# Kernel optimization log

Hardware: AMD Instinct MI355X
Metric: run time of the kernel (lower is better)

## Reference

```python
import jax, jax.numpy as jnp
import numpy as np

N = 100000      # nodes
E = 1600000     # edges (avg degree 16)
D_IN = 128
D_OUT = 128
P = 0.5         # dropout prob (module is in training mode)


def setup_inputs() -> dict:
    key = jax.random.key(0)
    k1, k2, k3 = jax.random.split(key, 3)
    x = jax.random.normal(k1, (N, D_IN), dtype=jnp.float32)
    edge_index = jax.random.randint(k2, (2, E), 0, N, dtype=jnp.int32)
    # GCNConv learned params (glorot-ish weight, zero bias)
    weight = jax.random.normal(k3, (D_IN, D_OUT), dtype=jnp.float32) / np.float32(np.sqrt(D_IN))
    bias = jnp.zeros((D_OUT,), dtype=jnp.float32)
    return {"x": x, "edge_index": edge_index, "weight": weight, "bias": bias}


def reference(x, edge_index, weight, bias):
    # --- GCNConv: add self-loops, symmetric deg^-1/2 normalization ---
    loops = jnp.arange(N, dtype=edge_index.dtype)
    src = jnp.concatenate([edge_index[0], loops])   # [E+N]
    dst = jnp.concatenate([edge_index[1], loops])   # [E+N]
    deg = jax.ops.segment_sum(jnp.ones_like(dst, dtype=x.dtype), dst, num_segments=N)
    dinv = jnp.where(deg > 0, jax.lax.rsqrt(deg), 0.0)          # deg^-1/2
    norm = dinv[src] * dinv[dst]                                # [E+N]
    h = x @ weight                                              # [N, D_OUT]
    msgs = h[src] * norm[:, None]                               # gather + scale
    out = jax.ops.segment_sum(msgs, dst, num_segments=N) + bias # scatter-add
    # --- ReLU ---
    out = jax.nn.relu(out)
    # --- Dropout (training=True), fixed key for determinism ---
    keep = jax.random.bernoulli(jax.random.key(42), 1.0 - P, out.shape)
    return jnp.where(keep, out / (1.0 - P), jnp.zeros((), out.dtype))
```

## Files before the change

### kernel.cpp

```cpp
#include <hip/hip_runtime.h>

#define N_NODES 100000
#define E_EDGES 1600000
#define D 128
#define PAD 136
#define GEMM_BLKS 1563
#define CCHUNK 4096
#define CNT_BLKS ((E_EDGES + CCHUNK - 1) / CCHUNK)
#define SCHUNK 4096
#define SCAT_BLKS ((E_EDGES + SCHUNK - 1) / SCHUNK)
#define RANGE 98
#define NR 1024
#define CAP 2048
#define NPW 13

typedef __attribute__((ext_vector_type(8))) short short8;
typedef __attribute__((ext_vector_type(8))) unsigned short ushort8v;
typedef __attribute__((ext_vector_type(4))) float f32x4;

__device__ __forceinline__ unsigned int rotl32(unsigned int x, int r) {
  return (x << r) | (x >> (32 - r));
}

__device__ __forceinline__ unsigned int threefry_bits(unsigned int ctr) {
  const unsigned int ks0 = 0u, ks1 = 42u;
  const unsigned int ks2 = ks0 ^ ks1 ^ 0x1BD11BDAu;
  unsigned int x0 = ks0;
  unsigned int x1 = ctr + ks1;
#define TF_ROUND(R) { x0 += x1; x1 = rotl32(x1, R); x1 ^= x0; }
  TF_ROUND(13) TF_ROUND(15) TF_ROUND(26) TF_ROUND(6)
  x0 += ks1; x1 += ks2 + 1u;
  TF_ROUND(17) TF_ROUND(29) TF_ROUND(16) TF_ROUND(24)
  x0 += ks2; x1 += ks0 + 2u;
  TF_ROUND(13) TF_ROUND(15) TF_ROUND(26) TF_ROUND(6)
  x0 += ks0; x1 += ks1 + 3u;
  TF_ROUND(17) TF_ROUND(29) TF_ROUND(16) TF_ROUND(24)
  x0 += ks1; x1 += ks2 + 4u;
  TF_ROUND(13) TF_ROUND(15) TF_ROUND(26) TF_ROUND(6)
  x0 += ks2; x1 += ks0 + 5u;
#undef TF_ROUND
  return x0 ^ x1;
}

__device__ __forceinline__ unsigned short f2bf(float f) {
  unsigned int u = __float_as_uint(f);
  u = (u + 0x7FFFu + ((u >> 16) & 1u)) >> 16;
  return (unsigned short)u;
}
__device__ __forceinline__ float bf2f_lo(unsigned int v) {
  return __uint_as_float(v << 16);
}
__device__ __forceinline__ float bf2f_hi(unsigned int v) {
  return __uint_as_float(v & 0xFFFF0000u);
}

__global__ __launch_bounds__(256) void k_init(const float* __restrict__ w,
                                              unsigned short* __restrict__ wbf,
                                              int* __restrict__ bnt) {
  int t = blockIdx.x * 256 + threadIdx.x;
  if (t < 128 * 128) {
    int k = t >> 7;
    int n = t & 127;
    wbf[n * 128 + k] = f2bf(w[t]);
  }
  if (t < NR) bnt[t] = 0;
}

__global__ __launch_bounds__(256) void k_gc(const float* __restrict__ x,
                                            const unsigned short* __restrict__ wbf,
                                            unsigned short* __restrict__ h,
                                            const int* __restrict__ ei,
                                            int* __restrict__ bnt) {
  __shared__ unsigned short Wl[128 * PAD];
  __shared__ unsigned short Xl[64 * PAD];
  const int t = threadIdx.x;

  if (blockIdx.x >= GEMM_BLKS) {
    int* lc = (int*)Xl;
    const int base = (blockIdx.x - GEMM_BLKS) * CCHUNK;
    for (int i = t; i < NR; i += 256) lc[i] = 0;
    __syncthreads();
#pragma unroll
    for (int i = 0; i < CCHUNK / 256; ++i) {
      int e = base + i * 256 + t;
      if (e < E_EDGES) {
        int d = ei[E_EDGES + e];
        atomicAdd(&lc[d / RANGE], 1);
      }
    }
    __syncthreads();
    for (int i = t; i < NR; i += 256) {
      int c = lc[i];
      if (c) atomicAdd(&bnt[i], c);
    }
    return;
  }

  const int row0 = blockIdx.x * 64;

#pragma unroll
  for (int i = 0; i < 8; ++i) {
    int u  = t + i * 256;
    int kg = u & 15;
    int n  = u >> 4;
    *(ushort8v*)&Wl[n * PAD + kg * 8] = *(const ushort8v*)&wbf[n * 128 + kg * 8];
  }
  const float4* x4 = (const float4*)x;
#pragma unroll
  for (int i = 0; i < 8; ++i) {
    int id = t + i * 256;
    int r  = id >> 5;
    int c4 = id & 31;
    int row = row0 + r; if (row >= N_NODES) row = N_NODES - 1;
    float4 v = x4[(long long)row * 32 + c4];
    ushort4 p;
    p.x = f2bf(v.x); p.y = f2bf(v.y); p.z = f2bf(v.z); p.w = f2bf(v.w);
    *(ushort4*)&Xl[r * PAD + c4 * 4] = p;
  }
  __syncthreads();

  const int wv   = t >> 6;
  const int l    = t & 63;
  const int quad = l >> 4;
  const int ln16 = l & 15;
  const int m0   = wv * 16;

  short8 a[4];
#pragma unroll
  for (int kt = 0; kt < 4; ++kt)
    a[kt] = *(const short8*)&Xl[(m0 + ln16) * PAD + kt * 32 + quad * 8];

#pragma unroll
  for (int nt = 0; nt < 8; ++nt) {
    f32x4 acc = {0.f, 0.f, 0.f, 0.f};
#pragma unroll
    for (int kt = 0; kt < 4; ++kt) {
      short8 b = *(const short8*)&Wl[(nt * 16 + ln16) * PAD + kt * 32 + quad * 8];
      acc = __builtin_amdgcn_mfma_f32_16x16x32_bf16(a[kt], b, acc, 0, 0, 0);
    }
#pragma unroll
    for (int r = 0; r < 4; ++r)
      Xl[(m0 + quad * 4 + r) * PAD + nt * 16 + ln16] = f2bf(acc[r]);
  }

#pragma unroll
  for (int v = 0; v < 4; ++v) {
    int idx = v * 64 + l;
    int rr  = idx >> 4;
    int ch  = idx & 15;
    int row = row0 + m0 + rr;
    if (row < N_NODES)
      *(ushort8v*)&h[(long long)row * D + ch * 8] = *(const ushort8v*)&Xl[(m0 + rr) * PAD + ch * 8];
  }
}

__global__ __launch_bounds__(1024) void k_scanb(const int* __restrict__ bnt,
                                                int* __restrict__ base,
                                                int* __restrict__ cur) {
  __shared__ int sm[NR];
  int t = threadIdx.x;
  int v = bnt[t];
  sm[t] = v;
  __syncthreads();
  for (int off = 1; off < NR; off <<= 1) {
    int x = (t >= off) ? sm[t - off] : 0;
    __syncthreads();
    sm[t] += x;
    __syncthreads();
  }
  int excl = sm[t] - v;
  base[t] = excl;
  cur[t]  = excl;
  if (t == NR - 1) base[NR] = sm[NR - 1];
}

__global__ __launch_bounds__(512) void k_scatter(const int* __restrict__ ei,
                                                 int* __restrict__ cur,
                                                 int* __restrict__ ebuf) {
  __shared__ int lcnt[NR];
  __shared__ int gbase[NR];
  const int t = threadIdx.x;
  const int base = blockIdx.x * SCHUNK;
  for (int i = t; i < NR; i += 512) lcnt[i] = 0;
  __syncthreads();
  int myb[SCHUNK / 512];
  int myr[SCHUNK / 512];
  int mypk[SCHUNK / 512];
#pragma unroll
  for (int i = 0; i < SCHUNK / 512; ++i) {
    int e = base + i * 512 + t;
    myb[i] = -1;
    if (e < E_EDGES) {
      int d = ei[E_EDGES + e];
      int s = ei[e];
      int b = d / RANGE;
      int dl = d - b * RANGE;
      myb[i]  = b;
      mypk[i] = s | (dl << 17);
      myr[i]  = atomicAdd(&lcnt[b], 1);
    }
  }
  __syncthreads();
  for (int i = t; i < NR; i += 512) {
    int c = lcnt[i];
    gbase[i] = c ? atomicAdd(&cur[i], c) : 0;
  }
  __syncthreads();
#pragma unroll
  for (int i = 0; i < SCHUNK / 512; ++i)
    if (myb[i] >= 0) ebuf[gbase[myb[i]] + myr[i]] = mypk[i];
}

__global__ __launch_bounds__(256) void k_deg(const int* __restrict__ ebuf,
                                             const int* __restrict__ base,
                                             float* __restrict__ dinv) {
  __shared__ int hist[RANGE];
  const int t = threadIdx.x;
  const int r = blockIdx.x;
  if (t < RANGE) hist[t] = 0;
  __syncthreads();
  const int lo = base[r], hi = base[r + 1];
  for (int e = lo + t; e < hi; e += 256)
    atomicAdd(&hist[((unsigned)ebuf[e]) >> 17], 1);
  __syncthreads();
  if (t < RANGE) {
    int n = r * RANGE + t;
    if (n < N_NODES) dinv[n] = rsqrtf((float)(hist[t] + 1));
  }
}

__global__ __launch_bounds__(512) void k_agg(const int* __restrict__ ebuf,
                                             const int* __restrict__ base,
                                             const float* __restrict__ dinv,
                                             const unsigned short* __restrict__ h,
                                             const float* __restrict__ bias,
                                             float* __restrict__ out) {
  __shared__ int ssort[CAP];
  __shared__ int shist[128];
  __shared__ int sscn[128];
  __shared__ int scur[128];
  const int t  = threadIdx.x;
  const int r  = blockIdx.x;
  const int wv = t >> 6;
  const int l  = t & 63;
  const unsigned int* h32 = (const unsigned int*)h;

  float a0[NPW], a1[NPW];
#pragma unroll
  for (int j = 0; j < NPW; ++j) { a0[j] = 0.f; a1[j] = 0.f; }

  const int lo = base[r], hi = base[r + 1];

  for (int c0 = lo; c0 < hi; c0 += CAP) {
    const int m = min(CAP, hi - c0);
    if (t < 128) shist[t] = 0;
    __syncthreads();

    int pk0 = -1, pk1 = -1, pk2 = -1, pk3 = -1;
    {
      int i0 = t, i1 = t + 512, i2 = t + 1024, i3 = t + 1536;
      if (i0 < m) { pk0 = ebuf[c0 + i0]; atomicAdd(&shist[((unsigned)pk0) >> 17], 1); }
      if (i1 < m) { pk1 = ebuf[c0 + i1]; atomicAdd(&shist[((unsigned)pk1) >> 17], 1); }
      if (i2 < m) { pk2 = ebuf[c0 + i2]; atomicAdd(&shist[((unsigned)pk2) >> 17], 1); }
      if (i3 < m) { pk3 = ebuf[c0 + i3]; atomicAdd(&shist[((unsigned)pk3) >> 17], 1); }
    }
    __syncthreads();

    if (t < 128) sscn[t] = shist[t];
    __syncthreads();
    for (int off = 1; off < 128; off <<= 1) {
      int xv = (t < 128 && t >= off) ? sscn[t - off] : 0;
      __syncthreads();
      if (t < 128) sscn[t] += xv;
      __syncthreads();
    }
    if (t < 128) scur[t] = sscn[t] - shist[t];
    __syncthreads();

    if (pk0 != -1) ssort[atomicAdd(&scur[((unsigned)pk0) >> 17], 1)] = pk0;
    if (pk1 != -1) ssort[atomicAdd(&scur[((unsigned)pk1) >> 17], 1)] = pk1;
    if (pk2 != -1) ssort[atomicAdd(&scur[((unsigned)pk2) >> 17], 1)] = pk2;
    if (pk3 != -1) ssort[atomicAdd(&scur[((unsigned)pk3) >> 17], 1)] = pk3;
    __syncthreads();

#pragma unroll
    for (int j = 0; j < NPW; ++j) {
      int nl = wv + 8 * j;
      if (nl < RANGE) {
        int s1i = sscn[nl];
        int s0i = s1i - shist[nl];
        float aa0 = a0[j], aa1 = a1[j];
#pragma unroll 4
        for (int e = s0i; e < s1i; ++e) {
          int p = ssort[e];
          int s = p & 0x1FFFF;
          float wgt = dinv[s];
          unsigned u = h32[(long long)s * 64 + l];
          aa0 = fmaf(bf2f_lo(u), wgt, aa0);
          aa1 = fmaf(bf2f_hi(u), wgt, aa1);
        }
        a0[j] = aa0; a1[j] = aa1;
      }
    }
    __syncthreads();
  }

#pragma unroll
  for (int j = 0; j < NPW; ++j) {
    int nl = wv + 8 * j;
    if (nl >= RANGE) continue;
    int n = r * RANGE + nl;
    if (n >= N_NODES) continue;
    float dv = dinv[n];
    unsigned hv = h32[(long long)n * 64 + l];
    float v0 = (a0[j] + bf2f_lo(hv) * dv) * dv;
    float v1 = (a1[j] + bf2f_hi(hv) * dv) * dv;
    float2 bb = ((const float2*)bias)[l];
    float r0 = fmaxf(v0 + bb.x, 0.f);
    float r1 = fmaxf(v1 + bb.y, 0.f);
    unsigned i0 = (unsigned)n * 128u + (unsigned)(2 * l);
    unsigned b0 = threefry_bits(i0);
    unsigned b1 = threefry_bits(i0 + 1u);
    float2 res;
    res.x = (b0 & 0x80000000u) ? 0.0f : r0 * 2.0f;
    res.y = (b1 & 0x80000000u) ? 0.0f : r1 * 2.0f;
    ((float2*)out)[(long long)n * 64 + l] = res;
  }
}

extern "C" void kernel_launch(void* const* d_in, const int* in_sizes, int n_in,
                              void* d_out, int out_size, void* d_ws, size_t ws_size,
                              hipStream_t stream) {
  const float* x    = (const float*)d_in[0];
  const int*   ei   = (const int*)d_in[1];
  const float* w    = (const float*)d_in[2];
  const float* bias = (const float*)d_in[3];
  float* out = (float*)d_out;

  char* p = (char*)d_ws;
  unsigned short* h   = (unsigned short*)p;  p += (size_t)N_NODES * D * 2;
  unsigned short* wbf = (unsigned short*)p;  p += 128 * 128 * 2;
  float* dinv = (float*)p;                   p += (size_t)(NR * RANGE) * 4;
  int* bnt    = (int*)p;                     p += NR * 4;
  int* base   = (int*)p;                     p += (NR + 4) * 4;
  int* cur    = (int*)p;                     p += NR * 4;
  int* ebuf   = (int*)p;                     p += (size_t)E_EDGES * 4;

  k_init<<<64, 256, 0, stream>>>(w, wbf, bnt);
  k_gc<<<GEMM_BLKS + CNT_BLKS, 256, 0, stream>>>(x, wbf, h, ei, bnt);
  k_scanb<<<1, NR, 0, stream>>>(bnt, base, cur);
  k_scatter<<<SCAT_BLKS, 512, 0, stream>>>(ei, cur, ebuf);
  k_deg<<<NR, 256, 0, stream>>>(ebuf, base, dinv);
  k_agg<<<NR, 512, 0, stream>>>(ebuf, base, dinv, h, bias, out);
}
```

Measured before the change: 246.6 us.

## Halve node bucket range, pad bucket counters, and shrink aggregation blocks

Node buckets shrink from 98 to 49 nodes, so there are twice as many buckets (2048). The aggregation kernel now uses 256-thread blocks with a 1024-entry sort buffer, giving more, smaller blocks for better load balance and occupancy. Global bucket counters are padded to a 16-int stride so atomics on different buckets no longer share a cache line. The sort buffer also stores pre-masked source indices so the inner loop skips the mask. The costs are more global atomics per counting block, and a scan that now handles two buckets per thread.

```diff
diff --git a/kernel.cpp b/kernel.cpp
--- a/kernel.cpp
+++ b/kernel.cpp
@@ -9,10 +9,11 @@
 #define CNT_BLKS ((E_EDGES + CCHUNK - 1) / CCHUNK)
 #define SCHUNK 4096
 #define SCAT_BLKS ((E_EDGES + SCHUNK - 1) / SCHUNK)
-#define RANGE 98
-#define NR 1024
-#define CAP 2048
+#define RANGE 49
+#define NR 2048
+#define CAP 1024
 #define NPW 13
+#define BST 16
 
 typedef __attribute__((ext_vector_type(8))) short short8;
 typedef __attribute__((ext_vector_type(8))) unsigned short ushort8v;
@@ -63,7 +64,7 @@
     int n = t & 127;
     wbf[n * 128 + k] = f2bf(w[t]);
   }
-  if (t < NR) bnt[t] = 0;
+  for (int i = t; i < NR * BST; i += 64 * 256) bnt[i] = 0;
 }
 
 __global__ __launch_bounds__(256) void k_gc(const float* __restrict__ x,
@@ -91,7 +92,7 @@
     __syncthreads();
     for (int i = t; i < NR; i += 256) {
       int c = lc[i];
-      if (c) atomicAdd(&bnt[i], c);
+      if (c) atomicAdd(&bnt[i * BST], c);
     }
     return;
   }
@@ -157,21 +158,25 @@
 __global__ __launch_bounds__(1024) void k_scanb(const int* __restrict__ bnt,
                                                 int* __restrict__ base,
                                                 int* __restrict__ cur) {
-  __shared__ int sm[NR];
+  __shared__ int sm[1024];
   int t = threadIdx.x;
-  int v = bnt[t];
-  sm[t] = v;
-  __syncthreads();
-  for (int off = 1; off < NR; off <<= 1) {
+  int v0 = bnt[(2 * t) * BST];
+  int v1 = bnt[(2 * t + 1) * BST];
+  int s = v0 + v1;
+  sm[t] = s;
+  __syncthreads();
+  for (int off = 1; off < 1024; off <<= 1) {
     int x = (t >= off) ? sm[t - off] : 0;
     __syncthreads();
     sm[t] += x;
     __syncthreads();
   }
-  int excl = sm[t] - v;
-  base[t] = excl;
-  cur[t]  = excl;
-  if (t == NR - 1) base[NR] = sm[NR - 1];
+  int excl = sm[t] - s;
+  base[2 * t]     = excl;
+  base[2 * t + 1] = excl + v0;
+  cur[(2 * t) * BST]     = excl;
+  cur[(2 * t + 1) * BST] = excl + v0;
+  if (t == 1023) base[NR] = sm[1023];
 }
 
 __global__ __launch_bounds__(512) void k_scatter(const int* __restrict__ ei,
@@ -203,7 +208,7 @@
   __syncthreads();
   for (int i = t; i < NR; i += 512) {
     int c = lcnt[i];
-    gbase[i] = c ? atomicAdd(&cur[i], c) : 0;
+    gbase[i] = c ? atomicAdd(&cur[i * BST], c) : 0;
   }
   __syncthreads();
 #pragma unroll
@@ -214,10 +219,10 @@
 __global__ __launch_bounds__(256) void k_deg(const int* __restrict__ ebuf,
                                              const int* __restrict__ base,
                                              float* __restrict__ dinv) {
-  __shared__ int hist[RANGE];
+  __shared__ int hist[64];
   const int t = threadIdx.x;
   const int r = blockIdx.x;
-  if (t < RANGE) hist[t] = 0;
+  if (t < 64) hist[t] = 0;
   __syncthreads();
   const int lo = base[r], hi = base[r + 1];
   for (int e = lo + t; e < hi; e += 256)
@@ -229,16 +234,16 @@
   }
 }
 
-__global__ __launch_bounds__(512) void k_agg(const int* __restrict__ ebuf,
+__global__ __launch_bounds__(256) void k_agg(const int* __restrict__ ebuf,
                                              const int* __restrict__ base,
                                              const float* __restrict__ dinv,
                                              const unsigned short* __restrict__ h,
                                              const float* __restrict__ bias,
                                              float* __restrict__ out) {
   __shared__ int ssort[CAP];
-  __shared__ int shist[128];
-  __shared__ int sscn[128];
-  __shared__ int scur[128];
+  __shared__ int shist[64];
+  __shared__ int sscn[64];
+  __shared__ int scur[64];
   const int t  = threadIdx.x;
   const int r  = blockIdx.x;
   const int wv = t >> 6;
@@ -253,12 +258,12 @@
 
   for (int c0 = lo; c0 < hi; c0 += CAP) {
     const int m = min(CAP, hi - c0);
-    if (t < 128) shist[t] = 0;
+    if (t < 64) shist[t] = 0;
     __syncthreads();
 
     int pk0 = -1, pk1 = -1, pk2 = -1, pk3 = -1;
     {
-      int i0 = t, i1 = t + 512, i2 = t + 1024, i3 = t + 1536;
+      int i0 = t, i1 = t + 256, i2 = t + 512, i3 = t + 768;
       if (i0 < m) { pk0 = ebuf[c0 + i0]; atomicAdd(&shist[((unsigned)pk0) >> 17], 1); }
       if (i1 < m) { pk1 = ebuf[c0 + i1]; atomicAdd(&shist[((unsigned)pk1) >> 17], 1); }
       if (i2 < m) { pk2 = ebuf[c0 + i2]; atomicAdd(&shist[((unsigned)pk2) >> 17], 1); }
@@ -266,34 +271,33 @@
     }
     __syncthreads();
 
-    if (t < 128) sscn[t] = shist[t];
-    __syncthreads();
-    for (int off = 1; off < 128; off <<= 1) {
-      int xv = (t < 128 && t >= off) ? sscn[t - off] : 0;
+    if (t < 64) sscn[t] = shist[t];
+    __syncthreads();
+    for (int off = 1; off < 64; off <<= 1) {
+      int xv = (t < 64 && t >= off) ? sscn[t - off] : 0;
       __syncthreads();
-      if (t < 128) sscn[t] += xv;
+      if (t < 64) sscn[t] += xv;
       __syncthreads();
     }
-    if (t < 128) scur[t] = sscn[t] - shist[t];
-    __syncthreads();
-
-    if (pk0 != -1) ssort[atomicAdd(&scur[((unsigned)pk0) >> 17], 1)] = pk0;
-    if (pk1 != -1) ssort[atomicAdd(&scur[((unsigned)pk1) >> 17], 1)] = pk1;
-    if (pk2 != -1) ssort[atomicAdd(&scur[((unsigned)pk2) >> 17], 1)] = pk2;
-    if (pk3 != -1) ssort[atomicAdd(&scur[((unsigned)pk3) >> 17], 1)] = pk3;
+    if (t < 64) scur[t] = sscn[t] - shist[t];
+    __syncthreads();
+
+    if (pk0 != -1) ssort[atomicAdd(&scur[((unsigned)pk0) >> 17], 1)] = pk0 & 0x1FFFF;
+    if (pk1 != -1) ssort[atomicAdd(&scur[((unsigned)pk1) >> 17], 1)] = pk1 & 0x1FFFF;
+    if (pk2 != -1) ssort[atomicAdd(&scur[((unsigned)pk2) >> 17], 1)] = pk2 & 0x1FFFF;
+    if (pk3 != -1) ssort[atomicAdd(&scur[((unsigned)pk3) >> 17], 1)] = pk3 & 0x1FFFF;
     __syncthreads();
 
 #pragma unroll
     for (int j = 0; j < NPW; ++j) {
-      int nl = wv + 8 * j;
+      int nl = wv + 4 * j;
       if (nl < RANGE) {
         int s1i = sscn[nl];
         int s0i = s1i - shist[nl];
         float aa0 = a0[j], aa1 = a1[j];
 #pragma unroll 4
         for (int e = s0i; e < s1i; ++e) {
-          int p = ssort[e];
-          int s = p & 0x1FFFF;
+          int s = ssort[e];
           float wgt = dinv[s];
           unsigned u = h32[(long long)s * 64 + l];
           aa0 = fmaf(bf2f_lo(u), wgt, aa0);
@@ -307,7 +311,7 @@
 
 #pragma unroll
   for (int j = 0; j < NPW; ++j) {
-    int nl = wv + 8 * j;
+    int nl = wv + 4 * j;
     if (nl >= RANGE) continue;
     int n = r * RANGE + nl;
     if (n >= N_NODES) continue;
@@ -341,15 +345,15 @@
   unsigned short* h   = (unsigned short*)p;  p += (size_t)N_NODES * D * 2;
   unsigned short* wbf = (unsigned short*)p;  p += 128 * 128 * 2;
   float* dinv = (float*)p;                   p += (size_t)(NR * RANGE) * 4;
-  int* bnt    = (int*)p;                     p += NR * 4;
+  int* bnt    = (int*)p;                     p += (size_t)NR * BST * 4;
   int* base   = (int*)p;                     p += (NR + 4) * 4;
-  int* cur    = (int*)p;                     p += NR * 4;
+  int* cur    = (int*)p;                     p += (size_t)NR * BST * 4;
   int* ebuf   = (int*)p;                     p += (size_t)E_EDGES * 4;
 
   k_init<<<64, 256, 0, stream>>>(w, wbf, bnt);
   k_gc<<<GEMM_BLKS + CNT_BLKS, 256, 0, stream>>>(x, wbf, h, ei, bnt);
-  k_scanb<<<1, NR, 0, stream>>>(bnt, base, cur);
+  k_scanb<<<1, 1024, 0, stream>>>(bnt, base, cur);
   k_scatter<<<SCAT_BLKS, 512, 0, stream>>>(ei, cur, ebuf);
   k_deg<<<NR, 256, 0, stream>>>(ebuf, base, dinv);
-  k_agg<<<NR, 512, 0, stream>>>(ebuf, base, dinv, h, bias, out);
-}
+  k_agg<<<NR, 256, 0, stream>>>(ebuf, base, dinv, h, bias, out);
+}
```

Result: slower. 287.5 us (+16.6%).

## Use deterministic per-block bucket offsets and pre-gather dinv weights into LDS

Applied to the files above, without the earlier changes.

Replaces the global atomic bucket counters with a per-block count matrix that is exclusive-scanned per bucket, so the scatter gets deterministic write offsets without global atomics. The counting blocks move to the front of the combined GEMM/count grid. In aggregation, each edge's dinv[src] weight is loaded once during the histogram pass and stored next to the source index in LDS, which takes a dependent global load out of the inner gather loop; that loop's unroll goes from 4 to 8. The cost is an extra serial scan kernel that walks 391 rows of counts, plus twice the LDS per sorted entry.

```diff
diff --git a/kernel.cpp b/kernel.cpp
--- a/kernel.cpp
+++ b/kernel.cpp
@@ -5,10 +5,8 @@
 #define D 128
 #define PAD 136
 #define GEMM_BLKS 1563
-#define CCHUNK 4096
-#define CNT_BLKS ((E_EDGES + CCHUNK - 1) / CCHUNK)
-#define SCHUNK 4096
-#define SCAT_BLKS ((E_EDGES + SCHUNK - 1) / SCHUNK)
+#define CHUNK 4096
+#define CNT_BLKS ((E_EDGES + CHUNK - 1) / CHUNK)
 #define RANGE 98
 #define NR 1024
 #define CAP 2048
@@ -55,33 +53,30 @@
 }
 
 __global__ __launch_bounds__(256) void k_init(const float* __restrict__ w,
-                                              unsigned short* __restrict__ wbf,
-                                              int* __restrict__ bnt) {
+                                              unsigned short* __restrict__ wbf) {
   int t = blockIdx.x * 256 + threadIdx.x;
-  if (t < 128 * 128) {
-    int k = t >> 7;
-    int n = t & 127;
-    wbf[n * 128 + k] = f2bf(w[t]);
-  }
-  if (t < NR) bnt[t] = 0;
+  int k = t >> 7;
+  int n = t & 127;
+  wbf[n * 128 + k] = f2bf(w[t]);
 }
 
 __global__ __launch_bounds__(256) void k_gc(const float* __restrict__ x,
                                             const unsigned short* __restrict__ wbf,
                                             unsigned short* __restrict__ h,
                                             const int* __restrict__ ei,
-                                            int* __restrict__ bnt) {
+                                            int* __restrict__ cnt) {
   __shared__ unsigned short Wl[128 * PAD];
   __shared__ unsigned short Xl[64 * PAD];
   const int t = threadIdx.x;
 
-  if (blockIdx.x >= GEMM_BLKS) {
+  if (blockIdx.x < CNT_BLKS) {
     int* lc = (int*)Xl;
-    const int base = (blockIdx.x - GEMM_BLKS) * CCHUNK;
+    const int B = blockIdx.x;
+    const int base = B * CHUNK;
     for (int i = t; i < NR; i += 256) lc[i] = 0;
     __syncthreads();
 #pragma unroll
-    for (int i = 0; i < CCHUNK / 256; ++i) {
+    for (int i = 0; i < CHUNK / 256; ++i) {
       int e = base + i * 256 + t;
       if (e < E_EDGES) {
         int d = ei[E_EDGES + e];
@@ -89,14 +84,11 @@
       }
     }
     __syncthreads();
-    for (int i = t; i < NR; i += 256) {
-      int c = lc[i];
-      if (c) atomicAdd(&bnt[i], c);
-    }
+    for (int i = t; i < NR; i += 256) cnt[B * NR + i] = lc[i];
     return;
   }
 
-  const int row0 = blockIdx.x * 64;
+  const int row0 = (blockIdx.x - CNT_BLKS) * 64;
 
 #pragma unroll
   for (int i = 0; i < 8; ++i) {
@@ -154,12 +146,24 @@
   }
 }
 
-__global__ __launch_bounds__(1024) void k_scanb(const int* __restrict__ bnt,
-                                                int* __restrict__ base,
-                                                int* __restrict__ cur) {
+__global__ __launch_bounds__(256) void k_scanA(int* __restrict__ cnt,
+                                               int* __restrict__ tot) {
+  const int b = blockIdx.x * 256 + threadIdx.x;
+  int running = 0;
+#pragma unroll 4
+  for (int B = 0; B < CNT_BLKS; ++B) {
+    int v = cnt[B * NR + b];
+    cnt[B * NR + b] = running;
+    running += v;
+  }
+  tot[b] = running;
+}
+
+__global__ __launch_bounds__(1024) void k_scanB(const int* __restrict__ tot,
+                                                int* __restrict__ base) {
   __shared__ int sm[NR];
   int t = threadIdx.x;
-  int v = bnt[t];
+  int v = tot[t];
   sm[t] = v;
   __syncthreads();
   for (int off = 1; off < NR; off <<= 1) {
@@ -168,27 +172,27 @@
     sm[t] += x;
     __syncthreads();
   }
-  int excl = sm[t] - v;
-  base[t] = excl;
-  cur[t]  = excl;
+  base[t] = sm[t] - v;
   if (t == NR - 1) base[NR] = sm[NR - 1];
 }
 
 __global__ __launch_bounds__(512) void k_scatter(const int* __restrict__ ei,
-                                                 int* __restrict__ cur,
+                                                 const int* __restrict__ cnt,
+                                                 const int* __restrict__ base,
                                                  int* __restrict__ ebuf) {
   __shared__ int lcnt[NR];
   __shared__ int gbase[NR];
   const int t = threadIdx.x;
-  const int base = blockIdx.x * SCHUNK;
+  const int B = blockIdx.x;
+  const int e0 = B * CHUNK;
   for (int i = t; i < NR; i += 512) lcnt[i] = 0;
   __syncthreads();
-  int myb[SCHUNK / 512];
-  int myr[SCHUNK / 512];
-  int mypk[SCHUNK / 512];
-#pragma unroll
-  for (int i = 0; i < SCHUNK / 512; ++i) {
-    int e = base + i * 512 + t;
+  int myb[CHUNK / 512];
+  int myr[CHUNK / 512];
+  int mypk[CHUNK / 512];
+#pragma unroll
+  for (int i = 0; i < CHUNK / 512; ++i) {
+    int e = e0 + i * 512 + t;
     myb[i] = -1;
     if (e < E_EDGES) {
       int d = ei[E_EDGES + e];
@@ -201,23 +205,21 @@
     }
   }
   __syncthreads();
-  for (int i = t; i < NR; i += 512) {
-    int c = lcnt[i];
-    gbase[i] = c ? atomicAdd(&cur[i], c) : 0;
-  }
-  __syncthreads();
-#pragma unroll
-  for (int i = 0; i < SCHUNK / 512; ++i)
+  for (int i = t; i < NR; i += 512)
+    gbase[i] = base[i] + cnt[B * NR + i];
+  __syncthreads();
+#pragma unroll
+  for (int i = 0; i < CHUNK / 512; ++i)
     if (myb[i] >= 0) ebuf[gbase[myb[i]] + myr[i]] = mypk[i];
 }
 
 __global__ __launch_bounds__(256) void k_deg(const int* __restrict__ ebuf,
                                              const int* __restrict__ base,
                                              float* __restrict__ dinv) {
-  __shared__ int hist[RANGE];
+  __shared__ int hist[128];
   const int t = threadIdx.x;
   const int r = blockIdx.x;
-  if (t < RANGE) hist[t] = 0;
+  if (t < 128) hist[t] = 0;
   __syncthreads();
   const int lo = base[r], hi = base[r + 1];
   for (int e = lo + t; e < hi; e += 256)
@@ -235,7 +237,7 @@
                                              const unsigned short* __restrict__ h,
                                              const float* __restrict__ bias,
                                              float* __restrict__ out) {
-  __shared__ int ssort[CAP];
+  __shared__ int2 sswp[CAP];
   __shared__ int shist[128];
   __shared__ int sscn[128];
   __shared__ int scur[128];
@@ -257,12 +259,13 @@
     __syncthreads();
 
     int pk0 = -1, pk1 = -1, pk2 = -1, pk3 = -1;
+    float w0 = 0.f, w1 = 0.f, w2 = 0.f, w3 = 0.f;
     {
       int i0 = t, i1 = t + 512, i2 = t + 1024, i3 = t + 1536;
-      if (i0 < m) { pk0 = ebuf[c0 + i0]; atomicAdd(&shist[((unsigned)pk0) >> 17], 1); }
-      if (i1 < m) { pk1 = ebuf[c0 + i1]; atomicAdd(&shist[((unsigned)pk1) >> 17], 1); }
-      if (i2 < m) { pk2 = ebuf[c0 + i2]; atomicAdd(&shist[((unsigned)pk2) >> 17], 1); }
-      if (i3 < m) { pk3 = ebuf[c0 + i3]; atomicAdd(&shist[((unsigned)pk3) >> 17], 1); }
+      if (i0 < m) { pk0 = ebuf[c0 + i0]; w0 = dinv[pk0 & 0x1FFFF]; atomicAdd(&shist[((unsigned)pk0) >> 17], 1); }
+      if (i1 < m) { pk1 = ebuf[c0 + i1]; w1 = dinv[pk1 & 0x1FFFF]; atomicAdd(&shist[((unsigned)pk1) >> 17], 1); }
+      if (i2 < m) { pk2 = ebuf[c0 + i2]; w2 = dinv[pk2 & 0x1FFFF]; atomicAdd(&shist[((unsigned)pk2) >> 17], 1); }
+      if (i3 < m) { pk3 = ebuf[c0 + i3]; w3 = dinv[pk3 & 0x1FFFF]; atomicAdd(&shist[((unsigned)pk3) >> 17], 1); }
     }
     __syncthreads();
 
@@ -277,10 +280,10 @@
     if (t < 128) scur[t] = sscn[t] - shist[t];
     __syncthreads();
 
-    if (pk0 != -1) ssort[atomicAdd(&scur[((unsigned)pk0) >> 17], 1)] = pk0;
-    if (pk1 != -1) ssort[atomicAdd(&scur[((unsigned)pk1) >> 17], 1)] = pk1;
-    if (pk2 != -1) ssort[atomicAdd(&scur[((unsigned)pk2) >> 17], 1)] = pk2;
-    if (pk3 != -1) ssort[atomicAdd(&scur[((unsigned)pk3) >> 17], 1)] = pk3;
+    if (pk0 != -1) sswp[atomicAdd(&scur[((unsigned)pk0) >> 17], 1)] = make_int2(pk0 & 0x1FFFF, __float_as_int(w0));
+    if (pk1 != -1) sswp[atomicAdd(&scur[((unsigned)pk1) >> 17], 1)] = make_int2(pk1 & 0x1FFFF, __float_as_int(w1));
+    if (pk2 != -1) sswp[atomicAdd(&scur[((unsigned)pk2) >> 17], 1)] = make_int2(pk2 & 0x1FFFF, __float_as_int(w2));
+    if (pk3 != -1) sswp[atomicAdd(&scur[((unsigned)pk3) >> 17], 1)] = make_int2(pk3 & 0x1FFFF, __float_as_int(w3));
     __syncthreads();
 
 #pragma unroll
@@ -290,12 +293,11 @@
         int s1i = sscn[nl];
         int s0i = s1i - shist[nl];
         float aa0 = a0[j], aa1 = a1[j];
-#pragma unroll 4
+#pragma unroll 8
         for (int e = s0i; e < s1i; ++e) {
-          int p = ssort[e];
-          int s = p & 0x1FFFF;
-          float wgt = dinv[s];
-          unsigned u = h32[(long long)s * 64 + l];
+          int2 p = sswp[e];
+          float wgt = __int_as_float(p.y);
+          unsigned u = h32[(long long)p.x * 64 + l];
           aa0 = fmaf(bf2f_lo(u), wgt, aa0);
           aa1 = fmaf(bf2f_hi(u), wgt, aa1);
         }
@@ -341,15 +343,16 @@
   unsigned short* h   = (unsigned short*)p;  p += (size_t)N_NODES * D * 2;
   unsigned short* wbf = (unsigned short*)p;  p += 128 * 128 * 2;
   float* dinv = (float*)p;                   p += (size_t)(NR * RANGE) * 4;
-  int* bnt    = (int*)p;                     p += NR * 4;
+  int* cnt    = (int*)p;                     p += (size_t)CNT_BLKS * NR * 4;
+  int* tot    = (int*)p;                     p += NR * 4;
   int* base   = (int*)p;                     p += (NR + 4) * 4;
-  int* cur    = (int*)p;                     p += NR * 4;
   int* ebuf   = (int*)p;                     p += (size_t)E_EDGES * 4;
 
-  k_init<<<64, 256, 0, stream>>>(w, wbf, bnt);
-  k_gc<<<GEMM_BLKS + CNT_BLKS, 256, 0, stream>>>(x, wbf, h, ei, bnt);
-  k_scanb<<<1, NR, 0, stream>>>(bnt, base, cur);
-  k_scatter<<<SCAT_BLKS, 512, 0, stream>>>(ei, cur, ebuf);
+  k_init<<<64, 256, 0, stream>>>(w, wbf);
+  k_gc<<<GEMM_BLKS + CNT_BLKS, 256, 0, stream>>>(x, wbf, h, ei, cnt);
+  k_scanA<<<4, 256, 0, stream>>>(cnt, tot);
+  k_scanB<<<1, NR, 0, stream>>>(tot, base);
+  k_scatter<<<CNT_BLKS, 512, 0, stream>>>(ei, cnt, base, ebuf);
   k_deg<<<NR, 256, 0, stream>>>(ebuf, base, dinv);
   k_agg<<<NR, 512, 0, stream>>>(ebuf, base, dinv, h, bias, out);
 }
```

Result: slower. 288.4 us (+17.0%).

## Bucket edges by source octant and destination, prefetch dinv weights into shared

Applied to the files above, without the earlier changes.

The aggregation kernel now sorts each chunk of edges into 1024 buckets keyed by source-node octant and local destination node. Each block walks the octants in a staggered order starting from blockIdx&7, so concurrently running blocks gather h rows from different regions, which is meant to improve L2 locality of the gathers. The per-edge dinv[src] lookup moves into the load phase and is stored alongside the source index in shared memory. In exchange the scan widens to 1024 bins, shared memory use grows, and the per-node inner loop is split across eight octant passes with shorter trip counts and no unroll pragma.

```diff
diff --git a/kernel.cpp b/kernel.cpp
--- a/kernel.cpp
+++ b/kernel.cpp
@@ -13,6 +13,8 @@
 #define NR 1024
 #define CAP 2048
 #define NPW 13
+#define NB 1024
+#define OCTN 12500
 
 typedef __attribute__((ext_vector_type(8))) short short8;
 typedef __attribute__((ext_vector_type(8))) unsigned short ushort8v;
@@ -214,10 +216,10 @@
 __global__ __launch_bounds__(256) void k_deg(const int* __restrict__ ebuf,
                                              const int* __restrict__ base,
                                              float* __restrict__ dinv) {
-  __shared__ int hist[RANGE];
+  __shared__ int hist[128];
   const int t = threadIdx.x;
   const int r = blockIdx.x;
-  if (t < RANGE) hist[t] = 0;
+  if (t < 128) hist[t] = 0;
   __syncthreads();
   const int lo = base[r], hi = base[r + 1];
   for (int e = lo + t; e < hi; e += 256)
@@ -235,14 +237,15 @@
                                              const unsigned short* __restrict__ h,
                                              const float* __restrict__ bias,
                                              float* __restrict__ out) {
-  __shared__ int ssort[CAP];
-  __shared__ int shist[128];
-  __shared__ int sscn[128];
-  __shared__ int scur[128];
+  __shared__ int2 sswp[CAP];
+  __shared__ int shist[NB];
+  __shared__ int sscn[NB];
+  __shared__ int scur[NB];
   const int t  = threadIdx.x;
   const int r  = blockIdx.x;
   const int wv = t >> 6;
   const int l  = t & 63;
+  const int ostart = blockIdx.x & 7;
   const unsigned int* h32 = (const unsigned int*)h;
 
   float a0[NPW], a1[NPW];
@@ -253,53 +256,68 @@
 
   for (int c0 = lo; c0 < hi; c0 += CAP) {
     const int m = min(CAP, hi - c0);
-    if (t < 128) shist[t] = 0;
+    shist[t] = 0; shist[t + 512] = 0;
     __syncthreads();
 
     int pk0 = -1, pk1 = -1, pk2 = -1, pk3 = -1;
+    int bk0 = 0, bk1 = 0, bk2 = 0, bk3 = 0;
+    float w0 = 0.f, w1 = 0.f, w2 = 0.f, w3 = 0.f;
     {
       int i0 = t, i1 = t + 512, i2 = t + 1024, i3 = t + 1536;
-      if (i0 < m) { pk0 = ebuf[c0 + i0]; atomicAdd(&shist[((unsigned)pk0) >> 17], 1); }
-      if (i1 < m) { pk1 = ebuf[c0 + i1]; atomicAdd(&shist[((unsigned)pk1) >> 17], 1); }
-      if (i2 < m) { pk2 = ebuf[c0 + i2]; atomicAdd(&shist[((unsigned)pk2) >> 17], 1); }
-      if (i3 < m) { pk3 = ebuf[c0 + i3]; atomicAdd(&shist[((unsigned)pk3) >> 17], 1); }
-    }
-    __syncthreads();
-
-    if (t < 128) sscn[t] = shist[t];
-    __syncthreads();
-    for (int off = 1; off < 128; off <<= 1) {
-      int xv = (t < 128 && t >= off) ? sscn[t - off] : 0;
+      if (i0 < m) { pk0 = ebuf[c0 + i0]; int s = pk0 & 0x1FFFF; w0 = dinv[s];
+                    bk0 = ((s / OCTN) << 7) | (((unsigned)pk0) >> 17); atomicAdd(&shist[bk0], 1); }
+      if (i1 < m) { pk1 = ebuf[c0 + i1]; int s = pk1 & 0x1FFFF; w1 = dinv[s];
+                    bk1 = ((s / OCTN) << 7) | (((unsigned)pk1) >> 17); atomicAdd(&shist[bk1], 1); }
+      if (i2 < m) { pk2 = ebuf[c0 + i2]; int s = pk2 & 0x1FFFF; w2 = dinv[s];
+                    bk2 = ((s / OCTN) << 7) | (((unsigned)pk2) >> 17); atomicAdd(&shist[bk2], 1); }
+      if (i3 < m) { pk3 = ebuf[c0 + i3]; int s = pk3 & 0x1FFFF; w3 = dinv[s];
+                    bk3 = ((s / OCTN) << 7) | (((unsigned)pk3) >> 17); atomicAdd(&shist[bk3], 1); }
+    }
+    __syncthreads();
+
+    int h0 = shist[2 * t], h1 = shist[2 * t + 1];
+    int ps = h0 + h1;
+    scur[t] = ps;
+    __syncthreads();
+    for (int off = 1; off < 512; off <<= 1) {
+      int xv = (t >= off) ? scur[t - off] : 0;
       __syncthreads();
-      if (t < 128) sscn[t] += xv;
+      scur[t] += xv;
       __syncthreads();
     }
-    if (t < 128) scur[t] = sscn[t] - shist[t];
-    __syncthreads();
-
-    if (pk0 != -1) ssort[atomicAdd(&scur[((unsigned)pk0) >> 17], 1)] = pk0;
-    if (pk1 != -1) ssort[atomicAdd(&scur[((unsigned)pk1) >> 17], 1)] = pk1;
-    if (pk2 != -1) ssort[atomicAdd(&scur[((unsigned)pk2) >> 17], 1)] = pk2;
-    if (pk3 != -1) ssort[atomicAdd(&scur[((unsigned)pk3) >> 17], 1)] = pk3;
-    __syncthreads();
-
-#pragma unroll
-    for (int j = 0; j < NPW; ++j) {
-      int nl = wv + 8 * j;
-      if (nl < RANGE) {
-        int s1i = sscn[nl];
-        int s0i = s1i - shist[nl];
-        float aa0 = a0[j], aa1 = a1[j];
-#pragma unroll 4
-        for (int e = s0i; e < s1i; ++e) {
-          int p = ssort[e];
-          int s = p & 0x1FFFF;
-          float wgt = dinv[s];
-          unsigned u = h32[(long long)s * 64 + l];
-          aa0 = fmaf(bf2f_lo(u), wgt, aa0);
-          aa1 = fmaf(bf2f_hi(u), wgt, aa1);
+    int P = scur[t];
+    __syncthreads();
+    sscn[2 * t]     = P - h1;
+    sscn[2 * t + 1] = P;
+    scur[2 * t]     = P - ps;
+    scur[2 * t + 1] = P - h1;
+    __syncthreads();
+
+    if (pk0 != -1) sswp[atomicAdd(&scur[bk0], 1)] = make_int2(pk0 & 0x1FFFF, __float_as_int(w0));
+    if (pk1 != -1) sswp[atomicAdd(&scur[bk1], 1)] = make_int2(pk1 & 0x1FFFF, __float_as_int(w1));
+    if (pk2 != -1) sswp[atomicAdd(&scur[bk2], 1)] = make_int2(pk2 & 0x1FFFF, __float_as_int(w2));
+    if (pk3 != -1) sswp[atomicAdd(&scur[bk3], 1)] = make_int2(pk3 & 0x1FFFF, __float_as_int(w3));
+    __syncthreads();
+
+    for (int op = 0; op < 8; ++op) {
+      int oct = (ostart + op) & 7;
+#pragma unroll
+      for (int j = 0; j < NPW; ++j) {
+        int nl = wv + 8 * j;
+        if (nl < RANGE) {
+          int b   = (oct << 7) | nl;
+          int s1i = sscn[b];
+          int s0i = s1i - shist[b];
+          float aa0 = a0[j], aa1 = a1[j];
+          for (int e = s0i; e < s1i; ++e) {
+            int2 p = sswp[e];
+            float wgt = __int_as_float(p.y);
+            unsigned u = h32[(long long)p.x * 64 + l];
+            aa0 = fmaf(bf2f_lo(u), wgt, aa0);
+            aa1 = fmaf(bf2f_hi(u), wgt, aa1);
+          }
+          a0[j] = aa0; a1[j] = aa1;
         }
-        a0[j] = aa0; a1[j] = aa1;
       }
     }
     __syncthreads();
```

Result: slower. 334.4 us (+35.6%).
